# Kernel tuning notes

Measured on AMD Instinct MI355X. Metric: run time of the kernel, lower is better.

## Reference

```python
import jax, jax.numpy as jnp
import numpy as np

B, T, E, H, V = 64, 32, 512, 512, 10000


def setup_inputs() -> dict:
    key = jax.random.key(0)
    ks = jax.random.split(key, 8)
    s_e = 1.0 / np.sqrt(E)
    s_h = 1.0 / np.sqrt(H)
    return {
        "features": jax.random.normal(ks[0], (B, E), dtype=jnp.float32),
        "captions": jax.random.randint(ks[1], (B, T), 0, V, dtype=jnp.int64),
        "embed_W": jax.random.normal(ks[2], (V, E), dtype=jnp.float32) * 0.05,
        "W_ih": jax.random.normal(ks[3], (4 * H, E), dtype=jnp.float32) * s_e,
        "W_hh": jax.random.normal(ks[4], (4 * H, H), dtype=jnp.float32) * s_h,
        "b_ih": jnp.zeros((4 * H,), dtype=jnp.float32),
        "b_hh": jnp.zeros((4 * H,), dtype=jnp.float32),
        "fc_W": jax.random.normal(ks[5], (V, H), dtype=jnp.float32) * s_h,
        "fc_b": jnp.zeros((V,), dtype=jnp.float32),
    }


def reference(features, captions, embed_W, W_ih, W_hh, b_ih, b_hh, fc_W, fc_b):
    batch = features.shape[0]
    hidden = W_hh.shape[1]
    # Build per-step LSTM inputs: t=0 uses image features, t>=1 uses embed(captions[:, t]).
    # (captions_embed[:, 0] is unused, matching the original forward.)
    cap_emb = embed_W[captions]                      # [B, T, E]
    xs = jnp.concatenate([features[:, None, :], cap_emb[:, 1:, :]], axis=1)  # [B, T, E]
    xs = jnp.swapaxes(xs, 0, 1)                      # [T, B, E] time-major for scan

    # Precompute input-to-hidden projections for all timesteps (one big GEMM).
    x_proj = jnp.einsum('tbe,ge->tbg', xs, W_ih) + b_ih + b_hh  # [T, B, 4H]

    def step(carry, xp_t):
        h, c = carry
        gates = xp_t + h @ W_hh.T                    # [B, 4H]
        i, f, g, o = jnp.split(gates, 4, axis=-1)    # PyTorch gate order i,f,g,o
        c = jax.nn.sigmoid(f) * c + jax.nn.sigmoid(i) * jnp.tanh(g)
        h = jax.nn.sigmoid(o) * jnp.tanh(c)
        return (h, c), h

    h0 = jnp.zeros((batch, hidden), dtype=features.dtype)
    c0 = jnp.zeros((batch, hidden), dtype=features.dtype)
    _, h_seq = jax.lax.scan(step, (h0, c0), x_proj)  # [T, B, H]

    # Output projection across all timesteps in one GEMM.
    logits = jnp.einsum('tbh,vh->btv', h_seq, fc_W) + fc_b  # [B, T, V]
    return logits
```

## Files before the change

### kernel.cpp

```cpp
#include <hip/hip_runtime.h>
#include <hip/hip_bf16.h>
#include <stdint.h>

typedef __attribute__((ext_vector_type(8))) short short8;
typedef __attribute__((ext_vector_type(4))) float floatx4;
typedef unsigned long long ull;

#define AT_LD(p)    __hip_atomic_load((p), __ATOMIC_RELAXED, __HIP_MEMORY_SCOPE_AGENT)
#define AT_ST(p, v) __hip_atomic_store((p), (v), __ATOMIC_RELAXED, __HIP_MEMORY_SCOPE_AGENT)
#define AT_ADD(p, v) __hip_atomic_fetch_add((p), (v), __ATOMIC_RELAXED, __HIP_MEMORY_SCOPE_AGENT)

__device__ __forceinline__ floatx4 mfma_bf16(short8 a, short8 b, floatx4 c) {
  return __builtin_amdgcn_mfma_f32_16x16x32_bf16(a, b, c, 0, 0, 0);
}

__device__ __forceinline__ void cvt8_store(const float* __restrict__ src,
                                           __hip_bfloat16* __restrict__ dst) {
  float4 a = *(const float4*)src;
  float4 b = *(const float4*)(src + 4);
  __hip_bfloat16 t[8];
  t[0] = __float2bfloat16(a.x); t[1] = __float2bfloat16(a.y);
  t[2] = __float2bfloat16(a.z); t[3] = __float2bfloat16(a.w);
  t[4] = __float2bfloat16(b.x); t[5] = __float2bfloat16(b.y);
  t[6] = __float2bfloat16(b.z); t[7] = __float2bfloat16(b.w);
  *(uint4*)dst = *(const uint4*)t;
}

__device__ __forceinline__ short8 cvt8_frag(const float* __restrict__ src) {
  float4 a = *(const float4*)src;
  float4 b = *(const float4*)(src + 4);
  union { __hip_bfloat16 h[8]; short8 s; } u;
  u.h[0] = __float2bfloat16(a.x); u.h[1] = __float2bfloat16(a.y);
  u.h[2] = __float2bfloat16(a.z); u.h[3] = __float2bfloat16(a.w);
  u.h[4] = __float2bfloat16(b.x); u.h[5] = __float2bfloat16(b.y);
  u.h[6] = __float2bfloat16(b.z); u.h[7] = __float2bfloat16(b.w);
  return u.s;
}

__global__ __launch_bounds__(256, 1) void fused_all(
    const float* __restrict__ feat,
    const int*   __restrict__ caps,
    const float* __restrict__ emb,
    const float* __restrict__ Wih,
    const float* __restrict__ Whh,
    const float* __restrict__ bih,
    const float* __restrict__ bhh,
    const float* __restrict__ fcW,
    const float* __restrict__ fcb,
    float* __restrict__ xprj,
    __hip_bfloat16* __restrict__ hseq,
    unsigned* __restrict__ cnt,
    float* __restrict__ out) {
  __shared__ __align__(16) char sm[16 * 1024 + 16];
  const int tid = threadIdx.x;
  const int w = tid >> 6, l = tid & 63, lr = l & 15, lq = l >> 4;

  unsigned* aux    = cnt + 4096;
  unsigned* xcnt   = aux;
  unsigned* xfront = aux + 16 * 32;
  unsigned* tfront = aux + 17 * 32;
  unsigned* queue  = aux + 18 * 32;

  const bool i64 = (caps[1] == 0) & (caps[3] == 0) & (caps[5] == 0) &
                   (caps[7] == 0) & (caps[9] == 0) & (caps[11] == 0) &
                   (caps[13] == 0);

  if (blockIdx.x < 64) {
    const int bg = blockIdx.x >> 4;
    const int ug = blockIdx.x & 15;
    const int bl = tid >> 5, uu = tid & 31;
    float (*gbuf)[16][32] = (float (*)[16][32])sm;
    __hip_bfloat16 (*hbuf)[32] = (__hip_bfloat16 (*)[32])(sm + 8192);
    unsigned* xsh = (unsigned*)(sm + 16384);
    float c0 = 0.f, c1 = 0.f;

    short8 B0[16], B1[16];
    {
      const float* w0 = Whh + (size_t)(w * 512 + ug * 32 + lr) * 512 + lq * 8;
      const float* w1 = w0 + (size_t)16 * 512;
#pragma unroll
      for (int kk = 0; kk < 16; ++kk) {
        B0[kk] = cvt8_frag(w0 + kk * 32);
        B1[kk] = cvt8_frag(w1 + kk * 32);
      }
    }

    unsigned xseen = 0;
    for (int t = 0; t < 32; ++t) {
      if (xseen * 2 <= (unsigned)t) {
        if (tid == 0) {
          unsigned v;
          while ((v = AT_LD(xfront)) <= (unsigned)(t >> 1))
            __builtin_amdgcn_s_sleep(2);
          *xsh = v;
        }
        __syncthreads();
        xseen = *xsh;
        __syncthreads();
      }
      const float* xr0 = xprj + ((size_t)t * 64 + bg * 16 + bl) * 2048 + ug * 32 + uu;
      const float* xr1 = xr0 + (size_t)8 * 2048;
      float xi0 = AT_LD(xr0),        xf0 = AT_LD(xr0 + 512);
      float xg0 = AT_LD(xr0 + 1024), xo0 = AT_LD(xr0 + 1536);
      float xi1 = AT_LD(xr1),        xf1 = AT_LD(xr1 + 512);
      float xg1 = AT_LD(xr1 + 1024), xo1 = AT_LD(xr1 + 1536);

      floatx4 a0 = {}, a1 = {};
      if (t > 0) {
        if (tid == 0) {
          const unsigned* f = cnt + ((t - 1) * 4 + bg) * 32;
          while (AT_LD(f) < 16u) __builtin_amdgcn_s_sleep(1);
        }
        __syncthreads();
        const ull* hp = (const ull*)(hseq + (size_t)((t - 1) * 64 + bg * 16 + lr) * 512);
#pragma unroll
        for (int kk = 0; kk < 16; ++kk) {
          union { ull u[2]; short8 v; } hv;
          hv.u[0] = AT_LD(hp + kk * 8 + lq * 2);
          hv.u[1] = AT_LD(hp + kk * 8 + lq * 2 + 1);
          a0 = mfma_bf16(hv.v, B0[kk], a0);
          a1 = mfma_bf16(hv.v, B1[kk], a1);
        }
      }
#pragma unroll
      for (int r = 0; r < 4; ++r) {
        gbuf[w][lq * 4 + r][lr] = a0[r];
        gbuf[w][lq * 4 + r][16 + lr] = a1[r];
      }
      __syncthreads();
      {
        float gi = gbuf[0][bl][uu] + xi0, gf = gbuf[1][bl][uu] + xf0;
        float gg = gbuf[2][bl][uu] + xg0, go = gbuf[3][bl][uu] + xo0;
        float c = 1.f / (1.f + __expf(-gf)) * c0 + 1.f / (1.f + __expf(-gi)) * tanhf(gg);
        c0 = c;
        hbuf[bl][uu] = __float2bfloat16(1.f / (1.f + __expf(-go)) * tanhf(c));
      }
      {
        float gi = gbuf[0][bl + 8][uu] + xi1, gf = gbuf[1][bl + 8][uu] + xf1;
        float gg = gbuf[2][bl + 8][uu] + xg1, go = gbuf[3][bl + 8][uu] + xo1;
        float c = 1.f / (1.f + __expf(-gf)) * c1 + 1.f / (1.f + __expf(-gi)) * tanhf(gg);
        c1 = c;
        hbuf[bl + 8][uu] = __float2bfloat16(1.f / (1.f + __expf(-go)) * tanhf(c));
      }
      __syncthreads();
      if (tid < 128) {
        int r = tid >> 3, g = tid & 7;
        ull val = *(const ull*)(&hbuf[r][g * 4]);
        ull* dst = (ull*)(hseq + (size_t)(t * 64 + bg * 16 + r) * 512 + ug * 32) + g;
        AT_ST(dst, val);
      }
      __builtin_amdgcn_s_waitcnt(0);
      __syncthreads();
      if (tid == 0) AT_ADD(cnt + (t * 4 + bg) * 32, 1u);
    }
  } else if (blockIdx.x == 64) {
    if (tid == 0) {
      for (int ib = 0; ib < 16; ++ib) {
        while (AT_LD(xcnt + ib * 32) < 16u) __builtin_amdgcn_s_sleep(2);
        AT_ST(xfront, (unsigned)(ib + 1));
      }
      for (int t = 0; t < 32; ++t) {
        for (int bg = 0; bg < 4; ++bg) {
          const unsigned* f = cnt + (t * 4 + bg) * 32;
          while (AT_LD(f) < 16u) __builtin_amdgcn_s_sleep(8);
        }
        AT_ST(tfront, (unsigned)(t + 1));
      }
    }
  }

  __hip_bfloat16* As = (__hip_bfloat16*)sm;
  __hip_bfloat16* Bs = As + 128 * 32;
  int* nslot = (int*)(sm + 16384);
  const int wr = (w & 1) * 64, wc = (w >> 1) * 64;
  const int flatA0 = 0 * 256 + w * 64 + l, flatA1 = 1 * 256 + w * 64 + l;
  const int row0 = flatA0 >> 2, c80 = (flatA0 & 3) * 8;
  const int row1 = flatA1 >> 2, c81 = (flatA1 & 3) * 8;

  for (;;) {
    __syncthreads();
    if (tid == 0) *nslot = (int)AT_ADD(queue, 1u);
    __syncthreads();
    const int n = *nslot;
    if (n >= 256 + 16 * 79) break;

    if (n < 256) {
      const int ib = n >> 4, jb = n & 15;
      const float* sA[2];
      const float* sB[2];
      {
        const int rg0 = ib * 128 + row0, tt0 = rg0 >> 6, b0 = rg0 & 63;
        const int rg1 = ib * 128 + row1, tt1 = rg1 >> 6, b1v = rg1 & 63;
        if (tt0 == 0) sA[0] = feat + (size_t)b0 * 512 + c80;
        else {
          int idx = i64 ? caps[(size_t)(b0 * 32 + tt0) * 2] : caps[b0 * 32 + tt0];
          idx = idx < 0 ? 0 : (idx > 9999 ? 9999 : idx);
          sA[0] = emb + (size_t)idx * 512 + c80;
        }
        if (tt1 == 0) sA[1] = feat + (size_t)b1v * 512 + c81;
        else {
          int idx = i64 ? caps[(size_t)(b1v * 32 + tt1) * 2] : caps[b1v * 32 + tt1];
          idx = idx < 0 ? 0 : (idx > 9999 ? 9999 : idx);
          sA[1] = emb + (size_t)idx * 512 + c81;
        }
        sB[0] = Wih + (size_t)(jb * 128 + row0) * 512 + c80;
        sB[1] = Wih + (size_t)(jb * 128 + row1) * 512 + c81;
      }
      floatx4 acc[4][4] = {};
      for (int kt = 0; kt < 16; ++kt) {
        const int k0 = kt * 32;
        cvt8_store(sA[0] + k0, As + (size_t)flatA0 * 8);
        cvt8_store(sB[0] + k0, Bs + (size_t)flatA0 * 8);
        cvt8_store(sA[1] + k0, As + (size_t)flatA1 * 8);
        cvt8_store(sB[1] + k0, Bs + (size_t)flatA1 * 8);
        __syncthreads();
        short8 af[4], bfr[4];
#pragma unroll
        for (int mt = 0; mt < 4; ++mt)
          af[mt] = *(const short8*)(As + (wr + mt * 16 + lr) * 32 + lq * 8);
#pragma unroll
        for (int nt = 0; nt < 4; ++nt)
          bfr[nt] = *(const short8*)(Bs + (wc + nt * 16 + lr) * 32 + lq * 8);
#pragma unroll
        for (int mt = 0; mt < 4; ++mt)
#pragma unroll
          for (int nt = 0; nt < 4; ++nt)
            acc[mt][nt] = mfma_bf16(af[mt], bfr[nt], acc[mt][nt]);
        __syncthreads();
      }
#pragma unroll
      for (int mt = 0; mt < 4; ++mt) {
#pragma unroll
        for (int nt = 0; nt < 4; ++nt) {
          int col = jb * 128 + wc + nt * 16 + lr;
          float bias = bih[col] + bhh[col];
#pragma unroll
          for (int r = 0; r < 4; ++r) {
            int row = ib * 128 + wr + mt * 16 + lq * 4 + r;
            AT_ST(xprj + (size_t)row * 2048 + col, acc[mt][nt][r] + bias);
          }
        }
      }
      __builtin_amdgcn_s_waitcnt(0);
      __syncthreads();
      if (tid == 0) AT_ADD(xcnt + ib * 32, 1u);
    } else {
      const int m = n - 256;
      const int ib = m / 79, jb = m - ib * 79;
      if (tid == 0) {
        const unsigned need = (unsigned)(2 * ib + 2);
        while (AT_LD(tfront) < need) __builtin_amdgcn_s_sleep(16);
      }
      __syncthreads();
      int rb0 = jb * 128 + row0; if (rb0 > 9999) rb0 = 9999;
      int rb1 = jb * 128 + row1; if (rb1 > 9999) rb1 = 9999;
      const float* sB0 = fcW + (size_t)rb0 * 512 + c80;
      const float* sB1 = fcW + (size_t)rb1 * 512 + c81;
      const ull* sA0 = (const ull*)(hseq + (size_t)(ib * 128 + row0) * 512 + c80);
      const ull* sA1 = (const ull*)(hseq + (size_t)(ib * 128 + row1) * 512 + c81);
      floatx4 acc[4][4] = {};
      for (int kt = 0; kt < 16; ++kt) {
        const int k0 = kt * 32;
        union { ull u[2]; uint4 q; } av;
        av.u[0] = AT_LD(sA0 + (k0 >> 2));
        av.u[1] = AT_LD(sA0 + (k0 >> 2) + 1);
        *(uint4*)(As + (size_t)flatA0 * 8) = av.q;
        cvt8_store(sB0 + k0, Bs + (size_t)flatA0 * 8);
        av.u[0] = AT_LD(sA1 + (k0 >> 2));
        av.u[1] = AT_LD(sA1 + (k0 >> 2) + 1);
        *(uint4*)(As + (size_t)flatA1 * 8) = av.q;
        cvt8_store(sB1 + k0, Bs + (size_t)flatA1 * 8);
        __syncthreads();
        short8 af[4], bfr[4];
#pragma unroll
        for (int mt = 0; mt < 4; ++mt)
          af[mt] = *(const short8*)(As + (wr + mt * 16 + lr) * 32 + lq * 8);
#pragma unroll
        for (int nt = 0; nt < 4; ++nt)
          bfr[nt] = *(const short8*)(Bs + (wc + nt * 16 + lr) * 32 + lq * 8);
#pragma unroll
        for (int mt = 0; mt < 4; ++mt)
#pragma unroll
          for (int nt = 0; nt < 4; ++nt)
            acc[mt][nt] = mfma_bf16(af[mt], bfr[nt], acc[mt][nt]);
        __syncthreads();
      }
#pragma unroll
      for (int mt = 0; mt < 4; ++mt) {
#pragma unroll
        for (int nt = 0; nt < 4; ++nt) {
          int col = jb * 128 + wc + nt * 16 + lr;
          if (col < 10000) {
            float bias = fcb[col];
#pragma unroll
            for (int r = 0; r < 4; ++r) {
              int row = ib * 128 + wr + mt * 16 + lq * 4 + r;
              size_t orow = (size_t)((row & 63) * 32 + (row >> 6));
              out[orow * 10000 + col] = acc[mt][nt][r] + bias;
            }
          }
        }
      }
    }
  }
}

extern "C" void kernel_launch(void* const* d_in, const int* in_sizes, int n_in,
                              void* d_out, int out_size, void* d_ws, size_t ws_size,
                              hipStream_t stream) {
  const float* feat = (const float*)d_in[0];
  const int* caps   = (const int*)d_in[1];
  const float* emb  = (const float*)d_in[2];
  const float* Wih  = (const float*)d_in[3];
  const float* Whh  = (const float*)d_in[4];
  const float* bih  = (const float*)d_in[5];
  const float* bhh  = (const float*)d_in[6];
  const float* fcW  = (const float*)d_in[7];
  const float* fcb  = (const float*)d_in[8];
  float* out = (float*)d_out;

  const size_t MB = 1048576;
  char* ws = (char*)d_ws;
  float*          xprj = (float*)(ws);
  __hip_bfloat16* hseq = (__hip_bfloat16*)(ws + 16 * MB);
  unsigned*       cnt  = (unsigned*)(ws + 18 * MB);

  hipMemsetAsync(cnt, 0, 32768, stream);

  fused_all<<<256, 256, 0, stream>>>(feat, caps, emb, Wih, Whh, bih, bhh,
                                     fcW, fcb, xprj, hseq, cnt, out);
}
```

Before: 342.2 us.

## Tag each hidden-state element with a timestep to replace counter-based step barriers

Each bf16 hidden value is stored in a 32-bit word together with a 16-bit tag holding the timestep. Consumers in the recurrence and in the output GEMM poll the data words themselves until every tag matches, instead of waiting on a per-step counter and a block-wide barrier. This removes the producer's store drain and syncthreads and the consumer's spin-then-sync on every step of the serial recurrence. In exchange the hidden-state buffer doubles in size, a larger 4 MB region must be zeroed each launch, and every load needs extra tag checks and repacking.

```diff
diff --git a/kernel.cpp b/kernel.cpp
--- a/kernel.cpp
+++ b/kernel.cpp
@@ -48,7 +48,7 @@
     const float* __restrict__ fcW,
     const float* __restrict__ fcb,
     float* __restrict__ xprj,
-    __hip_bfloat16* __restrict__ hseq,
+    unsigned* __restrict__ hseqT,
     unsigned* __restrict__ cnt,
     float* __restrict__ out) {
   __shared__ __align__(16) char sm[16 * 1024 + 16];
@@ -70,7 +70,7 @@
     const int ug = blockIdx.x & 15;
     const int bl = tid >> 5, uu = tid & 31;
     float (*gbuf)[16][32] = (float (*)[16][32])sm;
-    __hip_bfloat16 (*hbuf)[32] = (__hip_bfloat16 (*)[32])(sm + 8192);
+    unsigned short (*hbuf)[32] = (unsigned short (*)[32])(sm + 8192);
     unsigned* xsh = (unsigned*)(sm + 16384);
     float c0 = 0.f, c1 = 0.f;
 
@@ -107,19 +107,54 @@
 
       floatx4 a0 = {}, a1 = {};
       if (t > 0) {
-        if (tid == 0) {
-          const unsigned* f = cnt + ((t - 1) * 4 + bg) * 32;
-          while (AT_LD(f) < 16u) __builtin_amdgcn_s_sleep(1);
-        }
-        __syncthreads();
-        const ull* hp = (const ull*)(hseq + (size_t)((t - 1) * 64 + bg * 16 + lr) * 512);
+        const unsigned want = (unsigned)t;
+        const ull* hp = (const ull*)(hseqT +
+                          (size_t)((t - 1) * 64 + bg * 16 + lr) * 512) + lq * 4;
+        ull hA[16], hB[16], hC[16], hD[16];
+        unsigned okm = 0;
 #pragma unroll
         for (int kk = 0; kk < 16; ++kk) {
-          union { ull u[2]; short8 v; } hv;
-          hv.u[0] = AT_LD(hp + kk * 8 + lq * 2);
-          hv.u[1] = AT_LD(hp + kk * 8 + lq * 2 + 1);
-          a0 = mfma_bf16(hv.v, B0[kk], a0);
-          a1 = mfma_bf16(hv.v, B1[kk], a1);
+          hA[kk] = AT_LD(hp + kk * 16 + 0);
+          hB[kk] = AT_LD(hp + kk * 16 + 1);
+          hC[kk] = AT_LD(hp + kk * 16 + 2);
+          hD[kk] = AT_LD(hp + kk * 16 + 3);
+        }
+#pragma unroll
+        for (int kk = 0; kk < 16; ++kk) {
+          bool ok = ((((unsigned)hA[kk] ^ want) | ((unsigned)hB[kk] ^ want) |
+                      ((unsigned)hC[kk] ^ want) | ((unsigned)hD[kk] ^ want)) &
+                     0xFFFFu) == 0u;
+          okm |= (unsigned)__all(ok) << kk;
+        }
+        while (okm != 0xFFFFu) {
+          __builtin_amdgcn_s_sleep(1);
+#pragma unroll
+          for (int kk = 0; kk < 16; ++kk) {
+            if (!(okm & (1u << kk))) {
+              hA[kk] = AT_LD(hp + kk * 16 + 0);
+              hB[kk] = AT_LD(hp + kk * 16 + 1);
+              hC[kk] = AT_LD(hp + kk * 16 + 2);
+              hD[kk] = AT_LD(hp + kk * 16 + 3);
+              bool ok = ((((unsigned)hA[kk] ^ want) | ((unsigned)hB[kk] ^ want) |
+                          ((unsigned)hC[kk] ^ want) | ((unsigned)hD[kk] ^ want)) &
+                         0xFFFFu) == 0u;
+              okm |= (unsigned)__all(ok) << kk;
+            }
+          }
+        }
+#pragma unroll
+        for (int kk = 0; kk < 16; ++kk) {
+          union { unsigned short s[8]; short8 v; } fr;
+          fr.s[0] = (unsigned short)(hA[kk] >> 16);
+          fr.s[1] = (unsigned short)(hA[kk] >> 48);
+          fr.s[2] = (unsigned short)(hB[kk] >> 16);
+          fr.s[3] = (unsigned short)(hB[kk] >> 48);
+          fr.s[4] = (unsigned short)(hC[kk] >> 16);
+          fr.s[5] = (unsigned short)(hC[kk] >> 48);
+          fr.s[6] = (unsigned short)(hD[kk] >> 16);
+          fr.s[7] = (unsigned short)(hD[kk] >> 48);
+          a0 = mfma_bf16(fr.v, B0[kk], a0);
+          a1 = mfma_bf16(fr.v, B1[kk], a1);
         }
       }
 #pragma unroll
@@ -133,24 +168,26 @@
         float gg = gbuf[2][bl][uu] + xg0, go = gbuf[3][bl][uu] + xo0;
         float c = 1.f / (1.f + __expf(-gf)) * c0 + 1.f / (1.f + __expf(-gi)) * tanhf(gg);
         c0 = c;
-        hbuf[bl][uu] = __float2bfloat16(1.f / (1.f + __expf(-go)) * tanhf(c));
+        __hip_bfloat16 hb = __float2bfloat16(1.f / (1.f + __expf(-go)) * tanhf(c));
+        hbuf[bl][uu] = *(const unsigned short*)&hb;
       }
       {
         float gi = gbuf[0][bl + 8][uu] + xi1, gf = gbuf[1][bl + 8][uu] + xf1;
         float gg = gbuf[2][bl + 8][uu] + xg1, go = gbuf[3][bl + 8][uu] + xo1;
         float c = 1.f / (1.f + __expf(-gf)) * c1 + 1.f / (1.f + __expf(-gi)) * tanhf(gg);
         c1 = c;
-        hbuf[bl + 8][uu] = __float2bfloat16(1.f / (1.f + __expf(-go)) * tanhf(c));
+        __hip_bfloat16 hb = __float2bfloat16(1.f / (1.f + __expf(-go)) * tanhf(c));
+        hbuf[bl + 8][uu] = *(const unsigned short*)&hb;
       }
       __syncthreads();
-      if (tid < 128) {
-        int r = tid >> 3, g = tid & 7;
-        ull val = *(const ull*)(&hbuf[r][g * 4]);
-        ull* dst = (ull*)(hseq + (size_t)(t * 64 + bg * 16 + r) * 512 + ug * 32) + g;
-        AT_ST(dst, val);
-      }
-      __builtin_amdgcn_s_waitcnt(0);
-      __syncthreads();
+      {
+        const unsigned tagOut = (unsigned)(t + 1);
+        int r = tid >> 4, p = tid & 15;
+        unsigned lo = ((unsigned)hbuf[r][2 * p]     << 16) | tagOut;
+        unsigned hi = ((unsigned)hbuf[r][2 * p + 1] << 16) | tagOut;
+        ull val = ((ull)hi << 32) | (ull)lo;
+        AT_ST((ull*)(hseqT + (size_t)(t * 64 + bg * 16 + r) * 512 + ug * 32) + p, val);
+      }
       if (tid == 0) AT_ADD(cnt + (t * 4 + bg) * 32, 1u);
     }
   } else if (blockIdx.x == 64) {
@@ -256,20 +293,42 @@
       int rb1 = jb * 128 + row1; if (rb1 > 9999) rb1 = 9999;
       const float* sB0 = fcW + (size_t)rb0 * 512 + c80;
       const float* sB1 = fcW + (size_t)rb1 * 512 + c81;
-      const ull* sA0 = (const ull*)(hseq + (size_t)(ib * 128 + row0) * 512 + c80);
-      const ull* sA1 = (const ull*)(hseq + (size_t)(ib * 128 + row1) * 512 + c81);
+      const ull* pA0 = (const ull*)(hseqT + (size_t)(ib * 128 + row0) * 512 + c80);
+      const ull* pA1 = (const ull*)(hseqT + (size_t)(ib * 128 + row1) * 512 + c81);
+      const unsigned w0t = (unsigned)((ib * 128 + row0) >> 6) + 1;
+      const unsigned w1t = (unsigned)((ib * 128 + row1) >> 6) + 1;
       floatx4 acc[4][4] = {};
       for (int kt = 0; kt < 16; ++kt) {
-        const int k0 = kt * 32;
-        union { ull u[2]; uint4 q; } av;
-        av.u[0] = AT_LD(sA0 + (k0 >> 2));
-        av.u[1] = AT_LD(sA0 + (k0 >> 2) + 1);
-        *(uint4*)(As + (size_t)flatA0 * 8) = av.q;
-        cvt8_store(sB0 + k0, Bs + (size_t)flatA0 * 8);
-        av.u[0] = AT_LD(sA1 + (k0 >> 2));
-        av.u[1] = AT_LD(sA1 + (k0 >> 2) + 1);
-        *(uint4*)(As + (size_t)flatA1 * 8) = av.q;
-        cvt8_store(sB1 + k0, Bs + (size_t)flatA1 * 8);
+        const int o = kt * 16;
+        ull q0 = AT_LD(pA0 + o + 0), q1 = AT_LD(pA0 + o + 1);
+        ull q2 = AT_LD(pA0 + o + 2), q3 = AT_LD(pA0 + o + 3);
+        ull r0 = AT_LD(pA1 + o + 0), r1 = AT_LD(pA1 + o + 1);
+        ull r2 = AT_LD(pA1 + o + 2), r3 = AT_LD(pA1 + o + 3);
+        cvt8_store(sB0 + kt * 32, Bs + (size_t)flatA0 * 8);
+        cvt8_store(sB1 + kt * 32, Bs + (size_t)flatA1 * 8);
+        while (((((unsigned)q0 ^ w0t) | ((unsigned)q1 ^ w0t) |
+                 ((unsigned)q2 ^ w0t) | ((unsigned)q3 ^ w0t) |
+                 ((unsigned)r0 ^ w1t) | ((unsigned)r1 ^ w1t) |
+                 ((unsigned)r2 ^ w1t) | ((unsigned)r3 ^ w1t)) & 0xFFFFu) != 0u) {
+          __builtin_amdgcn_s_sleep(2);
+          q0 = AT_LD(pA0 + o + 0); q1 = AT_LD(pA0 + o + 1);
+          q2 = AT_LD(pA0 + o + 2); q3 = AT_LD(pA0 + o + 3);
+          r0 = AT_LD(pA1 + o + 0); r1 = AT_LD(pA1 + o + 1);
+          r2 = AT_LD(pA1 + o + 2); r3 = AT_LD(pA1 + o + 3);
+        }
+        {
+          union { unsigned short s[8]; uint4 u; } fa;
+          fa.s[0] = (unsigned short)(q0 >> 16); fa.s[1] = (unsigned short)(q0 >> 48);
+          fa.s[2] = (unsigned short)(q1 >> 16); fa.s[3] = (unsigned short)(q1 >> 48);
+          fa.s[4] = (unsigned short)(q2 >> 16); fa.s[5] = (unsigned short)(q2 >> 48);
+          fa.s[6] = (unsigned short)(q3 >> 16); fa.s[7] = (unsigned short)(q3 >> 48);
+          *(uint4*)(As + (size_t)flatA0 * 8) = fa.u;
+          fa.s[0] = (unsigned short)(r0 >> 16); fa.s[1] = (unsigned short)(r0 >> 48);
+          fa.s[2] = (unsigned short)(r1 >> 16); fa.s[3] = (unsigned short)(r1 >> 48);
+          fa.s[4] = (unsigned short)(r2 >> 16); fa.s[5] = (unsigned short)(r2 >> 48);
+          fa.s[6] = (unsigned short)(r3 >> 16); fa.s[7] = (unsigned short)(r3 >> 48);
+          *(uint4*)(As + (size_t)flatA1 * 8) = fa.u;
+        }
         __syncthreads();
         short8 af[4], bfr[4];
 #pragma unroll
@@ -321,12 +380,12 @@
 
   const size_t MB = 1048576;
   char* ws = (char*)d_ws;
-  float*          xprj = (float*)(ws);
-  __hip_bfloat16* hseq = (__hip_bfloat16*)(ws + 16 * MB);
-  unsigned*       cnt  = (unsigned*)(ws + 18 * MB);
-
-  hipMemsetAsync(cnt, 0, 32768, stream);
+  float*    xprj  = (float*)(ws);
+  unsigned* hseqT = (unsigned*)(ws + 16 * MB);
+  unsigned* cnt   = (unsigned*)(ws + 20 * MB);
+
+  hipMemsetAsync(ws + 16 * MB, 0, 4 * MB + 32768, stream);
 
   fused_all<<<256, 256, 0, stream>>>(feat, caps, emb, Wih, Whh, bih, bhh,
-                                     fcW, fcb, xprj, hseq, cnt, out);
-}
+                                     fcW, fcb, xprj, hseqT, cnt, out);
+}
```

Measured after the change: 439.7 us. 1.28x slower.

## Replace atomic step counters with per-block flags and write h directly from registers

Applied to the files above, without the earlier changes.

The per-step completion counter, which 16 blocks each incremented atomically, becomes 16 separate flags on padded lines. Each producer stores its own flag, and consumers sum all 16 with plain atomic loads. The hidden-state write-out also drops the LDS staging buffer and one barrier: lanes pair their bf16 values through a shuffle and store 32-bit words straight to global memory. The cost is more polling loads per wait, a much larger memset for the flag region, and narrower global stores.

```diff
diff --git a/kernel.cpp b/kernel.cpp
--- a/kernel.cpp
+++ b/kernel.cpp
@@ -55,7 +55,8 @@
   const int tid = threadIdx.x;
   const int w = tid >> 6, l = tid & 63, lr = l & 15, lq = l >> 4;
 
-  unsigned* aux    = cnt + 4096;
+  unsigned* flags  = cnt;
+  unsigned* aux    = cnt + 65536;
   unsigned* xcnt   = aux;
   unsigned* xfront = aux + 16 * 32;
   unsigned* tfront = aux + 17 * 32;
@@ -70,7 +71,6 @@
     const int ug = blockIdx.x & 15;
     const int bl = tid >> 5, uu = tid & 31;
     float (*gbuf)[16][32] = (float (*)[16][32])sm;
-    __hip_bfloat16 (*hbuf)[32] = (__hip_bfloat16 (*)[32])(sm + 8192);
     unsigned* xsh = (unsigned*)(sm + 16384);
     float c0 = 0.f, c1 = 0.f;
 
@@ -108,8 +108,14 @@
       floatx4 a0 = {}, a1 = {};
       if (t > 0) {
         if (tid == 0) {
-          const unsigned* f = cnt + ((t - 1) * 4 + bg) * 32;
-          while (AT_LD(f) < 16u) __builtin_amdgcn_s_sleep(1);
+          const unsigned* f = flags + (size_t)((t - 1) * 4 + bg) * 16 * 32;
+          for (;;) {
+            unsigned s = 0;
+#pragma unroll
+            for (int j = 0; j < 16; ++j) s += AT_LD(f + j * 32);
+            if (s == 16u) break;
+            __builtin_amdgcn_s_sleep(1);
+          }
         }
         __syncthreads();
         const ull* hp = (const ull*)(hseq + (size_t)((t - 1) * 64 + bg * 16 + lr) * 512);
@@ -128,30 +134,36 @@
         gbuf[w][lq * 4 + r][16 + lr] = a1[r];
       }
       __syncthreads();
+      unsigned h0b, h1b;
       {
         float gi = gbuf[0][bl][uu] + xi0, gf = gbuf[1][bl][uu] + xf0;
         float gg = gbuf[2][bl][uu] + xg0, go = gbuf[3][bl][uu] + xo0;
         float c = 1.f / (1.f + __expf(-gf)) * c0 + 1.f / (1.f + __expf(-gi)) * tanhf(gg);
         c0 = c;
-        hbuf[bl][uu] = __float2bfloat16(1.f / (1.f + __expf(-go)) * tanhf(c));
+        __hip_bfloat16 hb = __float2bfloat16(1.f / (1.f + __expf(-go)) * tanhf(c));
+        h0b = *(const unsigned short*)&hb;
       }
       {
         float gi = gbuf[0][bl + 8][uu] + xi1, gf = gbuf[1][bl + 8][uu] + xf1;
         float gg = gbuf[2][bl + 8][uu] + xg1, go = gbuf[3][bl + 8][uu] + xo1;
         float c = 1.f / (1.f + __expf(-gf)) * c1 + 1.f / (1.f + __expf(-gi)) * tanhf(gg);
         c1 = c;
-        hbuf[bl + 8][uu] = __float2bfloat16(1.f / (1.f + __expf(-go)) * tanhf(c));
-      }
-      __syncthreads();
-      if (tid < 128) {
-        int r = tid >> 3, g = tid & 7;
-        ull val = *(const ull*)(&hbuf[r][g * 4]);
-        ull* dst = (ull*)(hseq + (size_t)(t * 64 + bg * 16 + r) * 512 + ug * 32) + g;
-        AT_ST(dst, val);
+        __hip_bfloat16 hb = __float2bfloat16(1.f / (1.f + __expf(-go)) * tanhf(c));
+        h1b = *(const unsigned short*)&hb;
+      }
+      {
+        unsigned p0 = (unsigned)__shfl_xor((int)h0b, 1);
+        unsigned p1 = (unsigned)__shfl_xor((int)h1b, 1);
+        int row = bg * 16 + ((tid & 1) ? bl + 8 : bl);
+        unsigned word = (tid & 1) ? (p1 | (h1b << 16)) : (h0b | (p0 << 16));
+        unsigned* dst = (unsigned*)hseq + (size_t)(t * 64 + row) * 256 +
+                        ((ug * 32 + uu) >> 1);
+        AT_ST(dst, word);
       }
       __builtin_amdgcn_s_waitcnt(0);
       __syncthreads();
-      if (tid == 0) AT_ADD(cnt + (t * 4 + bg) * 32, 1u);
+      if (tid == 0)
+        AT_ST(flags + ((size_t)(t * 4 + bg) * 16 + ug) * 32, 1u);
     }
   } else if (blockIdx.x == 64) {
     if (tid == 0) {
@@ -161,8 +173,14 @@
       }
       for (int t = 0; t < 32; ++t) {
         for (int bg = 0; bg < 4; ++bg) {
-          const unsigned* f = cnt + (t * 4 + bg) * 32;
-          while (AT_LD(f) < 16u) __builtin_amdgcn_s_sleep(8);
+          const unsigned* f = flags + (size_t)(t * 4 + bg) * 16 * 32;
+          for (;;) {
+            unsigned s = 0;
+#pragma unroll
+            for (int j = 0; j < 16; ++j) s += AT_LD(f + j * 32);
+            if (s == 16u) break;
+            __builtin_amdgcn_s_sleep(8);
+          }
         }
         AT_ST(tfront, (unsigned)(t + 1));
       }
@@ -325,7 +343,7 @@
   __hip_bfloat16* hseq = (__hip_bfloat16*)(ws + 16 * MB);
   unsigned*       cnt  = (unsigned*)(ws + 18 * MB);
 
-  hipMemsetAsync(cnt, 0, 32768, stream);
+  hipMemsetAsync(cnt, 0, 512 * 1024, stream);
 
   fused_all<<<256, 256, 0, stream>>>(feat, caps, emb, Wih, Whh, bih, bhh,
                                      fcW, fcb, xprj, hseq, cnt, out);
```

Result: slower. 449.2 us (+31.2%).
